# Kernel tuning notes

Hardware: AMD Instinct MI355X
Metric: run time of the kernel (lower is better)

Reference implementation:

```python
import jax, jax.numpy as jnp
import numpy as np

N_NODES = 50000
N_EDGES = 800000
D = 256


def gcn_conv(x, edge_index, W, b, n_nodes):
    """PyG-style GCNConv: add self-loops, symmetric norm, linear, scatter-add."""
    # add self loops
    loops = jnp.arange(n_nodes, dtype=edge_index.dtype)
    src = jnp.concatenate([edge_index[0], loops])  # message sources
    dst = jnp.concatenate([edge_index[1], loops])  # aggregation targets
    # symmetric normalization: deg computed on targets (incl. self loops)
    deg = jax.ops.segment_sum(jnp.ones_like(dst, dtype=x.dtype), dst,
                              num_segments=n_nodes)
    dinv = jnp.where(deg > 0, jax.lax.rsqrt(deg), 0.0)
    norm = dinv[src] * dinv[dst]  # [E+N]
    h = x @ W  # [N, out]
    msg = h[src] * norm[:, None]  # gather + scale, [E+N, out]
    out = jax.ops.segment_sum(msg, dst, num_segments=n_nodes)  # scatter-add
    return out + b


def setup_inputs() -> dict:
    key = jax.random.key(0)
    k1, k2, k3, k4 = jax.random.split(key, 4)
    x = jax.random.normal(k1, (N_NODES, D), dtype=jnp.float32)
    edge_index = jax.random.randint(k2, (2, N_EDGES), 0, N_NODES, dtype=jnp.int64)
    s = 1.0 / np.sqrt(D)
    W1 = jax.random.normal(k3, (D, D), dtype=jnp.float32) * s
    W2 = jax.random.normal(k4, (D, D), dtype=jnp.float32) * s
    b1 = jnp.zeros((D,), dtype=jnp.float32)
    b2 = jnp.zeros((D,), dtype=jnp.float32)
    return {"x": x, "edge_index": edge_index, "W1": W1, "b1": b1,
            "W2": W2, "b2": b2}


def reference(x, edge_index, W1, b1, W2, b2):
    n = x.shape[0]
    out = gcn_conv(x, edge_index, W1, b1, n)
    out = jax.nn.relu(out)  # dropout is identity in eval mode (p=0.2 in train)
    out = out + gcn_conv(x, edge_index, W2, b2, n)
    return out
```

## Files before the change

kernel.cpp:

```cpp
#include <hip/hip_runtime.h>
#include <hip/hip_bf16.h>

#define DIM 256
#define CAP 64
#define GEMM_BX 64

typedef short bf16x8 __attribute__((ext_vector_type(8)));
typedef float f32x4  __attribute__((ext_vector_type(4)));
typedef unsigned int u32x4 __attribute__((ext_vector_type(4)));

__device__ __forceinline__ unsigned short f2b(float f) {
    union { __hip_bfloat16 h; unsigned short u; } cv;
    cv.h = __float2bfloat16(f);
    return cv.u;
}
__device__ __forceinline__ void acc8(u32x4 u, float* a) {
    a[0] += __uint_as_float(u.x << 16); a[1] += __uint_as_float(u.x & 0xffff0000u);
    a[2] += __uint_as_float(u.y << 16); a[3] += __uint_as_float(u.y & 0xffff0000u);
    a[4] += __uint_as_float(u.z << 16); a[5] += __uint_as_float(u.z & 0xffff0000u);
    a[6] += __uint_as_float(u.w << 16); a[7] += __uint_as_float(u.w & 0xffff0000u);
}

#define OFF_FILL   0
#define OFF_WT1    262144
#define OFF_WT2    393216
#define OFF_BUCKET 524288
#define OFF_AGG    6924544ull
#define OFF_YB     32524544ull
#define NEED_BF    (OFF_YB + 25600000ull)

__global__ void k_fill(const int* __restrict__ src, const int* __restrict__ dst,
                       int* __restrict__ fill, unsigned short* __restrict__ bucket, int nE) {
    int e = blockIdx.x * blockDim.x + threadIdx.x;
    if (e < nE) {
        int d = dst[e];
        int pos = atomicAdd(&fill[d], 1);
        if (pos < CAP) bucket[d * CAP + pos] = (unsigned short)src[e];
    }
}

__global__ void k_prep(const float* __restrict__ x, const int* __restrict__ fill,
                       u32x4* __restrict__ yb,
                       const float* __restrict__ W1, const float* __restrict__ W2,
                       unsigned short* __restrict__ wt1, unsigned short* __restrict__ wt2,
                       int nybBlocks, int n8) {
    if ((int)blockIdx.x < nybBlocks) {
        int t = blockIdx.x * 256 + threadIdx.x;
        if (t < n8) {
            int nN   = n8 >> 5;
            int s    = t / (nN * 4);
            int rest = t - s * (nN * 4);
            int node = rest >> 2;
            int ch   = rest & 3;
            int g    = s * 4 + ch;
            float d = rsqrtf((float)(1 + fill[node]));
            const f32x4* xp = (const f32x4*)x + ((size_t)node * 32 + g) * 2;
            f32x4 v0 = xp[0], v1 = xp[1];
            u32x4 r;
            r.x = (unsigned)f2b(d * v0.x) | ((unsigned)f2b(d * v0.y) << 16);
            r.y = (unsigned)f2b(d * v0.z) | ((unsigned)f2b(d * v0.w) << 16);
            r.z = (unsigned)f2b(d * v1.x) | ((unsigned)f2b(d * v1.y) << 16);
            r.w = (unsigned)f2b(d * v1.z) | ((unsigned)f2b(d * v1.w) << 16);
            yb[t] = r;
        }
    } else {
        int t = (blockIdx.x - nybBlocks) * 256 + threadIdx.x;
        if (t < DIM * DIM) {
            int k = t & 255, nn = t >> 8;
            wt1[t] = f2b(W1[k * DIM + nn]);
            wt2[t] = f2b(W2[k * DIM + nn]);
        }
    }
}

__global__ void k_agg_bf(const u32x4* __restrict__ yb, const int* __restrict__ fill,
                         const unsigned short* __restrict__ bucket,
                         u32x4* __restrict__ aggbf, int n) {
    int slice = blockIdx.x & 7;
    int nb    = blockIdx.x >> 3;
    int tid   = threadIdx.x;
    int wv    = tid >> 6;
    int lane  = tid & 63;
    int nd    = lane >> 5;
    int e     = (lane >> 2) & 7;
    int ch    = lane & 3;
    int node  = nb * 8 + wv * 2 + nd;
    bool valid = node < n;
    int nodeC = valid ? node : 0;

    const u32x4* ybs = yb + (size_t)slice * n * 4;

    int c = __builtin_nontemporal_load(&fill[nodeC]);
    float di = rsqrtf((float)(1 + c));
    if (c > CAP) c = CAP;
    const unsigned short* bk = bucket + (size_t)nodeC * CAP;

    unsigned short j0 = __builtin_nontemporal_load(bk + e);
    unsigned short j1 = __builtin_nontemporal_load(bk + e + 8);
    unsigned short j2 = __builtin_nontemporal_load(bk + e + 16);
    unsigned short j3 = __builtin_nontemporal_load(bk + e + 24);

    float a[8];
#pragma unroll
    for (int i = 0; i < 8; i++) a[i] = 0.f;

    if (e == 0)      acc8(ybs[(size_t)nodeC * 4 + ch], a);
    if (e < c)       acc8(ybs[(size_t)j0 * 4 + ch], a);
    if (e + 8 < c)   acc8(ybs[(size_t)j1 * 4 + ch], a);
    if (e + 16 < c)  acc8(ybs[(size_t)j2 * 4 + ch], a);
    if (e + 24 < c)  acc8(ybs[(size_t)j3 * 4 + ch], a);
    for (int k = 32 + e; k < c; k += 8) {
        unsigned short jj = __builtin_nontemporal_load(bk + k);
        acc8(ybs[(size_t)jj * 4 + ch], a);
    }

#pragma unroll
    for (int i = 0; i < 8; i++) a[i] += __shfl_xor(a[i], 4, 64);
#pragma unroll
    for (int i = 0; i < 8; i++) a[i] += __shfl_xor(a[i], 8, 64);
#pragma unroll
    for (int i = 0; i < 8; i++) a[i] += __shfl_xor(a[i], 16, 64);

    if (valid && e == 0) {
        u32x4 r;
        r.x = (unsigned)f2b(a[0] * di) | ((unsigned)f2b(a[1] * di) << 16);
        r.y = (unsigned)f2b(a[2] * di) | ((unsigned)f2b(a[3] * di) << 16);
        r.z = (unsigned)f2b(a[4] * di) | ((unsigned)f2b(a[5] * di) << 16);
        r.w = (unsigned)f2b(a[6] * di) | ((unsigned)f2b(a[7] * di) << 16);
        __builtin_nontemporal_store(r, &aggbf[(size_t)node * 32 + slice * 4 + ch]);
    }
}

__global__ void k_agg_f32(const float4* __restrict__ x4, const int* __restrict__ fill,
                          const unsigned short* __restrict__ bucket,
                          ushort4* __restrict__ aggbf, int n) {
    int node = (blockIdx.x * blockDim.x + threadIdx.x) >> 6;
    int lane = threadIdx.x & 63;
    if (node >= n) return;

    int c = fill[node];
    float di = rsqrtf((float)(1 + c));
    if (c > CAP) c = CAP;

    float4 xi = x4[(size_t)node * 64 + lane];
    float a0 = di * xi.x, a1 = di * xi.y, a2 = di * xi.z, a3 = di * xi.w;

    const unsigned short* bk = bucket + (size_t)node * CAP;
    for (int k = 0; k < c; k++) {
        int j = bk[k];
        float dj = rsqrtf((float)(1 + fill[j]));
        float4 xj = x4[(size_t)j * 64 + lane];
        a0 += dj * xj.x; a1 += dj * xj.y; a2 += dj * xj.z; a3 += dj * xj.w;
    }
    ushort4 r;
    r.x = f2b(a0 * di); r.y = f2b(a1 * di);
    r.z = f2b(a2 * di); r.w = f2b(a3 * di);
    aggbf[(size_t)node * 64 + lane] = r;
}

__launch_bounds__(256, 2)
__global__ void k_gemm(const short* __restrict__ aggbf,
                       const short* __restrict__ wt1, const short* __restrict__ wt2,
                       const float* __restrict__ b1, const float* __restrict__ b2,
                       float* __restrict__ out, int n, int ntiles) {
    __shared__ u32x4 bs[2048];

    int c0  = blockIdx.y * 32;
    int tid = threadIdx.x;

#pragma unroll
    for (int i = 0; i < 8; i++) {
        int l = tid + i * 256;
        int m = l >> 10, rem = l & 1023, nn = rem >> 5, p = rem & 31;
        const short* base = (m == 0) ? wt1 : wt2;
        const u32x4* sp = (const u32x4*)(base + (size_t)(c0 + nn) * DIM) + p;
        bs[(m << 10) + (nn << 5) + (p ^ nn)] = *sp;
    }
    __syncthreads();

    int lane = tid & 63;
    int wave = tid >> 6;
    int lrow = lane & 15;
    int quad = lane >> 4;

    bf16x8 w1r[2][8], w2r[2][8];
#pragma unroll
    for (int ct = 0; ct < 2; ct++) {
        int nn = ct * 16 + lrow;
#pragma unroll
        for (int s = 0; s < 8; s++) {
            int p = (4 * s + quad) ^ nn;
            u32x4 u = bs[(nn << 5) + p];
            u32x4 v = bs[1024 + (nn << 5) + p];
            __builtin_memcpy(&w1r[ct][s], &u, 16);
            __builtin_memcpy(&w2r[ct][s], &v, 16);
        }
    }

    f32x4 bb1[2], bb2[2];
#pragma unroll
    for (int ct = 0; ct < 2; ct++) {
        bb1[ct] = *(const f32x4*)&b1[c0 + ct * 16 + quad * 4];
        bb2[ct] = *(const f32x4*)&b2[c0 + ct * 16 + quad * 4];
    }

    for (int t = blockIdx.x; t < ntiles; t += gridDim.x) {
        int row = t * 64 + wave * 16 + lrow;
        int r = (row < n) ? row : 0;
        const short* ap = aggbf + (size_t)r * DIM + quad * 8;

        bf16x8 A[8];
#pragma unroll
        for (int s = 0; s < 8; s++) A[s] = *(const bf16x8*)(ap + s * 32);

        f32x4 acc1[2], acc2[2];
#pragma unroll
        for (int ct = 0; ct < 2; ct++) {
            acc1[ct] = (f32x4){0.f, 0.f, 0.f, 0.f};
            acc2[ct] = (f32x4){0.f, 0.f, 0.f, 0.f};
        }

#pragma unroll
        for (int s = 0; s < 8; s++) {
#pragma unroll
            for (int ct = 0; ct < 2; ct++) {
                acc1[ct] = __builtin_amdgcn_mfma_f32_16x16x32_bf16(w1r[ct][s], A[s], acc1[ct], 0, 0, 0);
                acc2[ct] = __builtin_amdgcn_mfma_f32_16x16x32_bf16(w2r[ct][s], A[s], acc2[ct], 0, 0, 0);
            }
        }

        if (row < n) {
#pragma unroll
            for (int ct = 0; ct < 2; ct++) {
                f32x4 v;
#pragma unroll
                for (int i = 0; i < 4; i++)
                    v[i] = fmaxf(acc1[ct][i] + bb1[ct][i], 0.f) + acc2[ct][i] + bb2[ct][i];
                f32x4* dstp = (f32x4*)&out[(size_t)row * DIM + c0 + ct * 16 + quad * 4];
                __builtin_nontemporal_store(v, dstp);
            }
        }
    }
}

extern "C" void kernel_launch(void* const* d_in, const int* in_sizes, int n_in,
                              void* d_out, int out_size, void* d_ws, size_t ws_size,
                              hipStream_t stream) {
    const float* x  = (const float*)d_in[0];
    const int*   ei = (const int*)d_in[1];
    const float* W1 = (const float*)d_in[2];
    const float* b1 = (const float*)d_in[3];
    const float* W2 = (const float*)d_in[4];
    const float* b2 = (const float*)d_in[5];
    float* out = (float*)d_out;

    int n = in_sizes[0] / DIM;
    int E = in_sizes[1] / 2;
    const int* src = ei;
    const int* dst = ei + E;

    char* ws = (char*)d_ws;
    int*            fill   = (int*)(ws + OFF_FILL);
    unsigned short* wt1    = (unsigned short*)(ws + OFF_WT1);
    unsigned short* wt2    = (unsigned short*)(ws + OFF_WT2);
    unsigned short* bucket = (unsigned short*)(ws + OFF_BUCKET);
    char*           aggp   = ws + OFF_AGG;
    u32x4*          yb     = (u32x4*)(ws + OFF_YB);

    (void)hipMemsetAsync(fill, 0, n * sizeof(int), stream);

    k_fill<<<(E + 255) / 256, 256, 0, stream>>>(src, dst, fill, bucket, E);

    bool use_bf = (ws_size >= NEED_BF);
    if (use_bf) {
        int n8 = n * (DIM / 8);
        int nybBlocks = (n8 + 255) / 256;
        k_prep<<<nybBlocks + 256, 256, 0, stream>>>(x, fill, yb, W1, W2, wt1, wt2,
                                                    nybBlocks, n8);
        int aggBlocks = ((n + 7) / 8) * 8;
        k_agg_bf<<<aggBlocks, 256, 0, stream>>>(yb, fill, bucket, (u32x4*)aggp, n);
    } else {
        k_prep<<<256, 256, 0, stream>>>(x, fill, yb, W1, W2, wt1, wt2, 0, 0);
        int aggBlocks = (n * 64 + 255) / 256;
        k_agg_f32<<<aggBlocks, 256, 0, stream>>>((const float4*)x, fill, bucket,
                                                 (ushort4*)aggp, n);
    }

    int ntiles = (n + 63) / 64;
    dim3 ggrid(GEMM_BX, DIM / 32);
    k_gemm<<<ggrid, 256, 0, stream>>>((const short*)aggp, (const short*)wt1,
                                      (const short*)wt2, b1, b2, out, n, ntiles);
}
```

Baseline: 276.5 us.

## Restructure bf16 aggregation to one 4-lane group per node with software-pipelined gathers

```diff
diff --git a/kernel.cpp b/kernel.cpp
--- a/kernel.cpp
+++ b/kernel.cpp
@@ -73,62 +73,98 @@
     }
 }
 
+__launch_bounds__(256, 4)
 __global__ void k_agg_bf(const u32x4* __restrict__ yb, const int* __restrict__ fill,
                          const unsigned short* __restrict__ bucket,
                          u32x4* __restrict__ aggbf, int n) {
     int slice = blockIdx.x & 7;
     int nb    = blockIdx.x >> 3;
     int tid   = threadIdx.x;
-    int wv    = tid >> 6;
-    int lane  = tid & 63;
-    int nd    = lane >> 5;
-    int e     = (lane >> 2) & 7;
-    int ch    = lane & 3;
-    int node  = nb * 8 + wv * 2 + nd;
-    bool valid = node < n;
-    int nodeC = valid ? node : 0;
+    int grp   = tid >> 2;
+    int ch    = tid & 3;
+    int node  = nb * 64 + grp;
+    if (node >= n) return;
 
     const u32x4* ybs = yb + (size_t)slice * n * 4;
 
-    int c = __builtin_nontemporal_load(&fill[nodeC]);
+    int c = __builtin_nontemporal_load(&fill[node]);
     float di = rsqrtf((float)(1 + c));
     if (c > CAP) c = CAP;
-    const unsigned short* bk = bucket + (size_t)nodeC * CAP;
-
-    unsigned short j0 = __builtin_nontemporal_load(bk + e);
-    unsigned short j1 = __builtin_nontemporal_load(bk + e + 8);
-    unsigned short j2 = __builtin_nontemporal_load(bk + e + 16);
-    unsigned short j3 = __builtin_nontemporal_load(bk + e + 24);
+    const unsigned short* bk = bucket + (size_t)node * CAP;
 
     float a[8];
 #pragma unroll
     for (int i = 0; i < 8; i++) a[i] = 0.f;
-
-    if (e == 0)      acc8(ybs[(size_t)nodeC * 4 + ch], a);
-    if (e < c)       acc8(ybs[(size_t)j0 * 4 + ch], a);
-    if (e + 8 < c)   acc8(ybs[(size_t)j1 * 4 + ch], a);
-    if (e + 16 < c)  acc8(ybs[(size_t)j2 * 4 + ch], a);
-    if (e + 24 < c)  acc8(ybs[(size_t)j3 * 4 + ch], a);
-    for (int k = 32 + e; k < c; k += 8) {
-        unsigned short jj = __builtin_nontemporal_load(bk + k);
-        acc8(ybs[(size_t)jj * 4 + ch], a);
-    }
-
-#pragma unroll
-    for (int i = 0; i < 8; i++) a[i] += __shfl_xor(a[i], 4, 64);
-#pragma unroll
-    for (int i = 0; i < 8; i++) a[i] += __shfl_xor(a[i], 8, 64);
-#pragma unroll
-    for (int i = 0; i < 8; i++) a[i] += __shfl_xor(a[i], 16, 64);
-
-    if (valid && e == 0) {
-        u32x4 r;
-        r.x = (unsigned)f2b(a[0] * di) | ((unsigned)f2b(a[1] * di) << 16);
-        r.y = (unsigned)f2b(a[2] * di) | ((unsigned)f2b(a[3] * di) << 16);
-        r.z = (unsigned)f2b(a[4] * di) | ((unsigned)f2b(a[5] * di) << 16);
-        r.w = (unsigned)f2b(a[6] * di) | ((unsigned)f2b(a[7] * di) << 16);
-        __builtin_nontemporal_store(r, &aggbf[(size_t)node * 32 + slice * 4 + ch]);
-    }
+    acc8(ybs[node * 4 + ch], a);
+
+#define EXTRACT8(iv, j) \
+    int j##0 = iv.x & 0xffff, j##1 = iv.x >> 16, j##2 = iv.y & 0xffff, j##3 = iv.y >> 16, \
+        j##4 = iv.z & 0xffff, j##5 = iv.z >> 16, j##6 = iv.w & 0xffff, j##7 = iv.w >> 16
+
+    int full = c & ~7;
+    if (full) {
+        u32x4 g[8], h[8];
+        u32x4 iv0 = *(const u32x4*)bk;
+        {
+            EXTRACT8(iv0, q);
+            g[0] = ybs[q0 * 4 + ch]; g[1] = ybs[q1 * 4 + ch];
+            g[2] = ybs[q2 * 4 + ch]; g[3] = ybs[q3 * 4 + ch];
+            g[4] = ybs[q4 * 4 + ch]; g[5] = ybs[q5 * 4 + ch];
+            g[6] = ybs[q6 * 4 + ch]; g[7] = ybs[q7 * 4 + ch];
+        }
+        u32x4 iv1 = *(const u32x4*)(bk + ((8 < full) ? 8 : 0));
+        for (int k = 8; k < full; k += 8) {
+            u32x4 ivn = *(const u32x4*)(bk + ((k + 8 < full) ? k + 8 : 0));
+            {
+                EXTRACT8(iv1, q);
+                h[0] = ybs[q0 * 4 + ch]; h[1] = ybs[q1 * 4 + ch];
+                h[2] = ybs[q2 * 4 + ch]; h[3] = ybs[q3 * 4 + ch];
+                h[4] = ybs[q4 * 4 + ch]; h[5] = ybs[q5 * 4 + ch];
+                h[6] = ybs[q6 * 4 + ch]; h[7] = ybs[q7 * 4 + ch];
+            }
+#pragma unroll
+            for (int i = 0; i < 8; i++) acc8(g[i], a);
+#pragma unroll
+            for (int i = 0; i < 8; i++) g[i] = h[i];
+            iv1 = ivn;
+        }
+#pragma unroll
+        for (int i = 0; i < 8; i++) acc8(g[i], a);
+    }
+
+    int rem = c - full;
+    if (rem) {
+        u32x4 iv = *(const u32x4*)(bk + full);
+        EXTRACT8(iv, q);
+        q1 = (rem > 1) ? q1 : 0;
+        q2 = (rem > 2) ? q2 : 0;
+        q3 = (rem > 3) ? q3 : 0;
+        q4 = (rem > 4) ? q4 : 0;
+        q5 = (rem > 5) ? q5 : 0;
+        q6 = (rem > 6) ? q6 : 0;
+        u32x4 r0 = ybs[q0 * 4 + ch];
+        u32x4 r1 = ybs[q1 * 4 + ch];
+        u32x4 r2 = ybs[q2 * 4 + ch];
+        u32x4 r3 = ybs[q3 * 4 + ch];
+        u32x4 r4 = ybs[q4 * 4 + ch];
+        u32x4 r5 = ybs[q5 * 4 + ch];
+        u32x4 r6 = ybs[q6 * 4 + ch];
+        acc8(r0, a);
+        if (rem > 1) acc8(r1, a);
+        if (rem > 2) acc8(r2, a);
+        if (rem > 3) acc8(r3, a);
+        if (rem > 4) acc8(r4, a);
+        if (rem > 5) acc8(r5, a);
+        if (rem > 6) acc8(r6, a);
+    }
+#undef EXTRACT8
+
+    u32x4 r;
+    r.x = (unsigned)f2b(a[0] * di) | ((unsigned)f2b(a[1] * di) << 16);
+    r.y = (unsigned)f2b(a[2] * di) | ((unsigned)f2b(a[3] * di) << 16);
+    r.z = (unsigned)f2b(a[4] * di) | ((unsigned)f2b(a[5] * di) << 16);
+    r.w = (unsigned)f2b(a[6] * di) | ((unsigned)f2b(a[7] * di) << 16);
+    __builtin_nontemporal_store(r, &aggbf[(size_t)node * 32 + slice * 4 + ch]);
 }
 
 __global__ void k_agg_f32(const float4* __restrict__ x4, const int* __restrict__ fill,
@@ -277,7 +313,7 @@
         int nybBlocks = (n8 + 255) / 256;
         k_prep<<<nybBlocks + 256, 256, 0, stream>>>(x, fill, yb, W1, W2, wt1, wt2,
                                                     nybBlocks, n8);
-        int aggBlocks = ((n + 7) / 8) * 8;
+        int aggBlocks = ((n + 63) / 64) * 8;
         k_agg_bf<<<aggBlocks, 256, 0, stream>>>(yb, fill, bucket, (u32x4*)aggp, n);
     } else {
         k_prep<<<256, 256, 0, stream>>>(x, fill, yb, W1, W2, wt1, wt2, 0, 0);
```

Result: faster. 239.2 us (-13.5%).
